# Optimization experiments

Hardware: AMD Instinct MI355X
Metric: run time of the kernel (lower is better)

Reference implementation:

```python
import jax, jax.numpy as jnp
import numpy as np

H, W = 4096, 4096
KH, KW = 11, 11


def setup_inputs() -> dict:
    key = jax.random.key(0)
    k1, k2 = jax.random.split(key)
    x = jax.random.normal(k1, (H, W), dtype=jnp.float32)
    weight = jax.random.uniform(k2, (KH, KW), dtype=jnp.float32)
    bias = jnp.zeros((1,), dtype=jnp.float32)
    return {"x": x, "weight": weight, "bias": bias}


def reference(x, weight, bias):
    # corr2d: valid 2D cross-correlation of a single-channel image with a
    # single kernel, then add scalar bias. Output shape [H-KH+1, W-KW+1].
    out = jax.lax.conv_general_dilated(
        x[None, None, :, :],            # NCHW, N=C=1
        weight[None, None, :, :],       # OIHW, O=I=1
        window_strides=(1, 1),
        padding="VALID",
        dimension_numbers=("NCHW", "OIHW", "NCHW"),
    )[0, 0]
    return out + bias[0]
```

## Files before the change

### kernel.cpp

```cpp
#include <hip/hip_runtime.h>
#include <hip/hip_bf16.h>

#define IH 4096
#define IW 4096
#define KH 11
#define KW 11
#define OH (IH - KH + 1)
#define OW (IW - KW + 1)

#define SROWS   26
#define TSTRIDE 84
#define NCHW    20
#define WCHUNK  (SROWS * NCHW)
#define TILE_SHORTS (SROWS * TSTRIDE)

#define STRIPS_X 64
#define ROWS_Y   256
#define NBLK     (STRIPS_X * ROWS_Y)

typedef short bf16x4 __attribute__((ext_vector_type(4)));
typedef short bf16x8 __attribute__((ext_vector_type(8)));
typedef float f32x4  __attribute__((ext_vector_type(4)));

__device__ __forceinline__ short f2b(float f) {
    __hip_bfloat16 h = __float2bfloat16(f);
    return __builtin_bit_cast(short, h);
}

__global__ void build_bmat(const float* __restrict__ w, short* __restrict__ bm) {
    const int tid = threadIdx.x;
#pragma unroll
    for (int t = 0; t < 22; ++t) {
        const int idx = tid + t * 256;
        const int kh = idx >> 9;
        const int j  = (idx >> 5) & 15;
        const int k  = idx & 31;
        const int d  = k - j;
        const float val = (d >= 0 && d < KW) ? w[kh * KW + d] : 0.f;
        bm[idx] = f2b(val);
    }
}

__global__ __launch_bounds__(64)
void conv2d_1w(const float* __restrict__ x,
               const short* __restrict__ bg,
               const float* __restrict__ bias,
               float* __restrict__ out) {
    __shared__ short tile[TILE_SHORTS];

    const int lane = threadIdx.x;
    const int g    = lane >> 4;
    const int li   = lane & 15;

    const int id    = (blockIdx.x & 7) * (NBLK / 8) + (blockIdx.x >> 3);
    const int strip = id >> 8;
    const int ty    = id & 255;
    const int gx0   = strip * 64;
    const int gy0   = ty * 16;

    const short* bp = bg + li * 32 + g * 8;
#define BLOAD(KH) const bf16x8 B##KH = *reinterpret_cast<const bf16x8*>(bp + (KH) * 512)
    BLOAD(0); BLOAD(1); BLOAD(2); BLOAD(3); BLOAD(4); BLOAD(5);
    BLOAD(6); BLOAD(7); BLOAD(8); BLOAD(9); BLOAD(10);
#undef BLOAD

#pragma unroll
    for (int it = 0; it < 9; ++it) {
        const int i = lane + it * 64;
        if (i < WCHUNK) {
            const int r  = i / NCHW;
            const int c4 = i - r * NCHW;
            const int gy = gy0 + r;
            const int gx = gx0 + c4 * 4;
            float4 v = make_float4(0.f, 0.f, 0.f, 0.f);
            if (gy < IH && gx + 3 < IW) {
                v = *reinterpret_cast<const float4*>(x + (size_t)gy * IW + gx);
            }
            bf16x4 b = { f2b(v.x), f2b(v.y), f2b(v.z), f2b(v.w) };
            *reinterpret_cast<bf16x4*>(&tile[r * TSTRIDE + c4 * 4]) = b;
        }
    }

    f32x4 acc[4] = {};
    const short* ap = &tile[li * TSTRIDE + g * 8];

    bf16x8 Ae[4], Ao[4];
#define LOADA(A, ROW) do {                                                   \
        const short* p_ = ap + (ROW) * TSTRIDE;                              \
        _Pragma("unroll")                                                    \
        for (int c = 0; c < 4; ++c) {                                        \
            bf16x4 lo = *reinterpret_cast<const bf16x4*>(p_ + c * 16);       \
            bf16x4 hi = *reinterpret_cast<const bf16x4*>(p_ + c * 16 + 4);   \
            A[c] = __builtin_shufflevector(lo, hi, 0, 1, 2, 3, 4, 5, 6, 7);  \
        }                                                                    \
    } while (0)
#define MFMA4(A, B) do {                                                     \
        _Pragma("unroll")                                                    \
        for (int c = 0; c < 4; ++c)                                          \
            acc[c] = __builtin_amdgcn_mfma_f32_16x16x32_bf16(A[c], B,        \
                                                             acc[c], 0, 0, 0); \
    } while (0)
#define STEPE(KH, B) LOADA(Ao, (KH) + 1); MFMA4(Ae, B); \
        __builtin_amdgcn_sched_barrier(0)
#define STEPO(KH, B) LOADA(Ae, (KH) + 1); MFMA4(Ao, B); \
        __builtin_amdgcn_sched_barrier(0)

    LOADA(Ae, 0);
    STEPE(0, B0);  STEPO(1, B1);  STEPE(2, B2);  STEPO(3, B3);
    STEPE(4, B4);  STEPO(5, B5);  STEPE(6, B6);  STEPO(7, B7);
    STEPE(8, B8);  STEPO(9, B9);  MFMA4(Ae, B10);

#undef STEPE
#undef STEPO
#undef MFMA4
#undef LOADA

    const float bv = bias[0];
#pragma unroll
    for (int c = 0; c < 4; ++c) {
        const int ox = gx0 + c * 16 + li;
        if (ox < OW) {
#pragma unroll
            for (int r = 0; r < 4; ++r) {
                const int oy = gy0 + g * 4 + r;
                if (oy < OH) {
                    out[(size_t)oy * OW + ox] = acc[c][r] + bv;
                }
            }
        }
    }
}

extern "C" void kernel_launch(void* const* d_in, const int* in_sizes, int n_in,
                              void* d_out, int out_size, void* d_ws, size_t ws_size,
                              hipStream_t stream) {
    const float* x    = (const float*)d_in[0];
    const float* w    = (const float*)d_in[1];
    const float* bias = (const float*)d_in[2];
    float* out        = (float*)d_out;
    short* bm         = (short*)d_ws;

    build_bmat<<<dim3(1), dim3(256), 0, stream>>>(w, bm);

    dim3 grid(NBLK);
    dim3 block(64);
    conv2d_1w<<<grid, block, 0, stream>>>(x, bm, bias, out);
}
```

Baseline: 44.37 us.

## Use async global-to-LDS loads with double-buffered 64x64 tiles per block

Replaces the one-wave 16-row strip kernel with 512-thread blocks that each process two adjacent 64x64 output tiles. Input rows are staged as fp32 directly into LDS with global_load_lds, and the second tile's load overlaps the first tile's MFMA compute. The bf16 conversion moves to the LDS read path. Larger tiles cut the halo re-read overhead (74 rows per 64 instead of 26 per 16), at the cost of twice the LDS footprint from fp32 storage, conversion work inside the inner loop, and fewer blocks overall.

Measured after the change: 40.43 us. 1.1x faster.

```diff
diff --git a/kernel.cpp b/kernel.cpp
--- a/kernel.cpp
+++ b/kernel.cpp
@@ -8,17 +8,17 @@
 #define OH (IH - KH + 1)
 #define OW (IW - KW + 1)
 
-#define SROWS   26
-#define TSTRIDE 84
-#define NCHW    20
-#define WCHUNK  (SROWS * NCHW)
-#define TILE_SHORTS (SROWS * TSTRIDE)
+#define BM 64
+#define BN 64
+#define TROWS   74
+#define FSTRIDE 84
+#define NCH_ROW 21
+#define NCHUNK  (TROWS * NCH_ROW)
+#define TILE_FLOATS (TROWS * FSTRIDE)
 
-#define STRIPS_X 64
-#define ROWS_Y   256
-#define NBLK     (STRIPS_X * ROWS_Y)
+#define TILES_X 64
+#define NPAIR   2048
 
-typedef short bf16x4 __attribute__((ext_vector_type(4)));
 typedef short bf16x8 __attribute__((ext_vector_type(8)));
 typedef float f32x4  __attribute__((ext_vector_type(4)));
 
@@ -41,94 +41,115 @@
     }
 }
 
-__global__ __launch_bounds__(64)
-void conv2d_1w(const float* __restrict__ x,
-               const short* __restrict__ bg,
-               const float* __restrict__ bias,
-               float* __restrict__ out) {
-    __shared__ short tile[TILE_SHORTS];
+__global__ __launch_bounds__(512)
+void conv2d_async(const float* __restrict__ x,
+                  const short* __restrict__ bg,
+                  const float* __restrict__ bias,
+                  float* __restrict__ out) {
+    __shared__ float buf[2][TILE_FLOATS];
 
-    const int lane = threadIdx.x;
+    const int tid = threadIdx.x;
+    const int pair = (blockIdx.x & 7) * (NPAIR / 8) + (blockIdx.x >> 3);
+    const int t0   = pair * 2;
+    const int gy0  = (t0 >> 6) * BM;
+    const int gxb  = (t0 & (TILES_X - 1)) * BN;
+
+    const int lane = tid & 63;
+    const int wvb  = tid & ~63;
+    const int wv   = tid >> 6;
+    const int wr   = wv >> 1;
+    const int ch   = wv & 1;
     const int g    = lane >> 4;
     const int li   = lane & 15;
-
-    const int id    = (blockIdx.x & 7) * (NBLK / 8) + (blockIdx.x >> 3);
-    const int strip = id >> 8;
-    const int ty    = id & 255;
-    const int gx0   = strip * 64;
-    const int gy0   = ty * 16;
+    const float bv = bias[0];
 
     const short* bp = bg + li * 32 + g * 8;
-#define BLOAD(KH) const bf16x8 B##KH = *reinterpret_cast<const bf16x8*>(bp + (KH) * 512)
+#define BLOAD(K) const bf16x8 B##K = *reinterpret_cast<const bf16x8*>(bp + (K) * 512)
     BLOAD(0); BLOAD(1); BLOAD(2); BLOAD(3); BLOAD(4); BLOAD(5);
     BLOAD(6); BLOAD(7); BLOAD(8); BLOAD(9); BLOAD(10);
 #undef BLOAD
 
-#pragma unroll
-    for (int it = 0; it < 9; ++it) {
-        const int i = lane + it * 64;
-        if (i < WCHUNK) {
-            const int r  = i / NCHW;
-            const int c4 = i - r * NCHW;
-            const int gy = gy0 + r;
-            const int gx = gx0 + c4 * 4;
-            float4 v = make_float4(0.f, 0.f, 0.f, 0.f);
-            if (gy < IH && gx + 3 < IW) {
-                v = *reinterpret_cast<const float4*>(x + (size_t)gy * IW + gx);
-            }
-            bf16x4 b = { f2b(v.x), f2b(v.y), f2b(v.z), f2b(v.w) };
-            *reinterpret_cast<bf16x4*>(&tile[r * TSTRIDE + c4 * 4]) = b;
-        }
-    }
-
-    f32x4 acc[4] = {};
-    const short* ap = &tile[li * TSTRIDE + g * 8];
-
-    bf16x8 Ae[4], Ao[4];
-#define LOADA(A, ROW) do {                                                   \
-        const short* p_ = ap + (ROW) * TSTRIDE;                              \
+#define DMAST(BI, GX0) do {                                                  \
         _Pragma("unroll")                                                    \
-        for (int c = 0; c < 4; ++c) {                                        \
-            bf16x4 lo = *reinterpret_cast<const bf16x4*>(p_ + c * 16);       \
-            bf16x4 hi = *reinterpret_cast<const bf16x4*>(p_ + c * 16 + 4);   \
-            A[c] = __builtin_shufflevector(lo, hi, 0, 1, 2, 3, 4, 5, 6, 7);  \
+        for (int it_ = 0; it_ < 4; ++it_) {                                  \
+            const int i_ = tid + it_ * 512;                                  \
+            if (i_ < NCHUNK) {                                               \
+                const int r_  = i_ / NCH_ROW;                                \
+                const int c4_ = i_ - r_ * NCH_ROW;                           \
+                const int gy_ = gy0 + r_;                                    \
+                const int gx_ = (GX0) + c4_ * 4;                             \
+                const float* s_ = (c4_ < 20 && gy_ < IH && gx_ + 3 < IW)     \
+                                  ? (x + (size_t)gy_ * IW + gx_) : x;        \
+                __builtin_amdgcn_global_load_lds(                            \
+                    (const __attribute__((address_space(1))) void*)s_,      \
+                    (__attribute__((address_space(3))) void*)                \
+                        &buf[BI][(it_ * 512 + wvb) * 4],                     \
+                    16, 0, 0);                                               \
+            }                                                                \
         }                                                                    \
     } while (0)
-#define MFMA4(A, B) do {                                                     \
+
+#define LOADA(A, ROW) do {                                                   \
         _Pragma("unroll")                                                    \
-        for (int c = 0; c < 4; ++c)                                          \
-            acc[c] = __builtin_amdgcn_mfma_f32_16x16x32_bf16(A[c], B,        \
-                                                             acc[c], 0, 0, 0); \
+        for (int c_ = 0; c_ < 2; ++c_) {                                     \
+            f32x4 p_ = *reinterpret_cast<const f32x4*>(ap + (ROW) * FSTRIDE + c_ * 16);     \
+            f32x4 q_ = *reinterpret_cast<const f32x4*>(ap + (ROW) * FSTRIDE + c_ * 16 + 4); \
+            bf16x8 v_;                                                       \
+            _Pragma("unroll")                                                \
+            for (int e_ = 0; e_ < 4; ++e_) {                                 \
+                v_[e_] = f2b(p_[e_]); v_[4 + e_] = f2b(q_[e_]);              \
+            }                                                                \
+            A[c_] = v_;                                                      \
+        }                                                                    \
     } while (0)
-#define STEPE(KH, B) LOADA(Ao, (KH) + 1); MFMA4(Ae, B); \
+#define MFMA2(A, BF) do {                                                    \
+        _Pragma("unroll")                                                    \
+        for (int c_ = 0; c_ < 2; ++c_)                                       \
+            acc[c_] = __builtin_amdgcn_mfma_f32_16x16x32_bf16(A[c_], (BF),   \
+                                                              acc[c_], 0, 0, 0); \
+    } while (0)
+#define STEPE(K, BF) LOADA(Ao, (K) + 1); MFMA2(Ae, BF); \
         __builtin_amdgcn_sched_barrier(0)
-#define STEPO(KH, B) LOADA(Ae, (KH) + 1); MFMA4(Ao, B); \
+#define STEPO(K, BF) LOADA(Ae, (K) + 1); MFMA2(Ao, BF); \
         __builtin_amdgcn_sched_barrier(0)
 
-    LOADA(Ae, 0);
-    STEPE(0, B0);  STEPO(1, B1);  STEPE(2, B2);  STEPO(3, B3);
-    STEPE(4, B4);  STEPO(5, B5);  STEPE(6, B6);  STEPO(7, B7);
-    STEPE(8, B8);  STEPO(9, B9);  MFMA4(Ae, B10);
+#define COMPUTE(BI, GX0) do {                                                \
+        f32x4 acc[2] = {};                                                   \
+        const float* ap = &buf[BI][(16 * wr + li) * FSTRIDE + ch * 32 + g * 8]; \
+        bf16x8 Ae[2], Ao[2];                                                 \
+        LOADA(Ae, 0);                                                        \
+        STEPE(0, B0); STEPO(1, B1); STEPE(2, B2); STEPO(3, B3);              \
+        STEPE(4, B4); STEPO(5, B5); STEPE(6, B6); STEPO(7, B7);              \
+        STEPE(8, B8); STEPO(9, B9); MFMA2(Ae, B10);                          \
+        _Pragma("unroll")                                                    \
+        for (int c_ = 0; c_ < 2; ++c_) {                                     \
+            const int ox_ = (GX0) + ch * 32 + c_ * 16 + li;                  \
+            if (ox_ < OW) {                                                  \
+                _Pragma("unroll")                                            \
+                for (int r_ = 0; r_ < 4; ++r_) {                             \
+                    const int oy_ = gy0 + wr * 16 + g * 4 + r_;              \
+                    if (oy_ < OH)                                            \
+                        out[(size_t)oy_ * OW + ox_] = acc[c_][r_] + bv;      \
+                }                                                            \
+            }                                                                \
+        }                                                                    \
+    } while (0)
 
+    DMAST(0, gxb);
+    __syncthreads();
+
+    DMAST(1, gxb + BN);
+    COMPUTE(0, gxb);
+    __syncthreads();
+
+    COMPUTE(1, gxb + BN);
+
+#undef COMPUTE
+#undef STEPO
 #undef STEPE
-#undef STEPO
-#undef MFMA4
+#undef MFMA2
 #undef LOADA
-
-    const float bv = bias[0];
-#pragma unroll
-    for (int c = 0; c < 4; ++c) {
-        const int ox = gx0 + c * 16 + li;
-        if (ox < OW) {
-#pragma unroll
-            for (int r = 0; r < 4; ++r) {
-                const int oy = gy0 + g * 4 + r;
-                if (oy < OH) {
-                    out[(size_t)oy * OW + ox] = acc[c][r] + bv;
-                }
-            }
-        }
-    }
+#undef DMAST
 }
 
 extern "C" void kernel_launch(void* const* d_in, const int* in_sizes, int n_in,
@@ -142,7 +163,7 @@
 
     build_bmat<<<dim3(1), dim3(256), 0, stream>>>(w, bm);
 
-    dim3 grid(NBLK);
-    dim3 block(64);
-    conv2d_1w<<<grid, block, 0, stream>>>(x, bm, bias, out);
+    dim3 grid(NPAIR);
+    dim3 block(512);
+    conv2d_async<<<grid, block, 0, stream>>>(x, bm, bias, out);
 }
```

## Share one 64x64 input tile across four waves to cut halo reloads

Applied to the files above, without the earlier changes.

Each block now has four waves that compute a 64x64 output tile from one shared bf16 staging tile of 74 rows, replacing single-wave 16-row strips that each reloaded a 10-row halo. This reduces redundant global reads of the input. The A-fragment pipeline switches to triple buffering with two rows prefetched ahead. It adds a block-wide barrier and larger blocks, which may reduce latency hiding per CU.

Measured after the change: 40.60 us. 8.5% less time.

```diff
diff --git a/kernel.cpp b/kernel.cpp
--- a/kernel.cpp
+++ b/kernel.cpp
@@ -8,15 +8,17 @@
 #define OH (IH - KH + 1)
 #define OW (IW - KW + 1)
 
-#define SROWS   26
+#define BM 64
+#define BN 64
+#define TROWS   74
 #define TSTRIDE 84
-#define NCHW    20
-#define WCHUNK  (SROWS * NCHW)
-#define TILE_SHORTS (SROWS * TSTRIDE)
+#define NC4     20
+#define NCHUNK  (TROWS * NC4)
+#define NITER   6
+#define TILE_SHORTS (TROWS * TSTRIDE)
 
-#define STRIPS_X 64
-#define ROWS_Y   256
-#define NBLK     (STRIPS_X * ROWS_Y)
+#define TILES_X 64
+#define NTILE   4096
 
 typedef short bf16x4 __attribute__((ext_vector_type(4)));
 typedef short bf16x8 __attribute__((ext_vector_type(8)));
@@ -41,35 +43,36 @@
     }
 }
 
-__global__ __launch_bounds__(64)
-void conv2d_1w(const float* __restrict__ x,
+__global__ __launch_bounds__(256)
+void conv2d_p3(const float* __restrict__ x,
                const short* __restrict__ bg,
                const float* __restrict__ bias,
                float* __restrict__ out) {
     __shared__ short tile[TILE_SHORTS];
 
-    const int lane = threadIdx.x;
+    const int tid = threadIdx.x;
+    const int blk = (blockIdx.x & 7) * (NTILE / 8) + (blockIdx.x >> 3);
+    const int gy0 = (blk >> 6) * BM;
+    const int gx0 = (blk & (TILES_X - 1)) * BN;
+
+    const int lane = tid & 63;
+    const int wv   = tid >> 6;
     const int g    = lane >> 4;
     const int li   = lane & 15;
-
-    const int id    = (blockIdx.x & 7) * (NBLK / 8) + (blockIdx.x >> 3);
-    const int strip = id >> 8;
-    const int ty    = id & 255;
-    const int gx0   = strip * 64;
-    const int gy0   = ty * 16;
+    const float bv = bias[0];
 
     const short* bp = bg + li * 32 + g * 8;
-#define BLOAD(KH) const bf16x8 B##KH = *reinterpret_cast<const bf16x8*>(bp + (KH) * 512)
+#define BLOAD(K) const bf16x8 B##K = *reinterpret_cast<const bf16x8*>(bp + (K) * 512)
     BLOAD(0); BLOAD(1); BLOAD(2); BLOAD(3); BLOAD(4); BLOAD(5);
     BLOAD(6); BLOAD(7); BLOAD(8); BLOAD(9); BLOAD(10);
 #undef BLOAD
 
 #pragma unroll
-    for (int it = 0; it < 9; ++it) {
-        const int i = lane + it * 64;
-        if (i < WCHUNK) {
-            const int r  = i / NCHW;
-            const int c4 = i - r * NCHW;
+    for (int it = 0; it < NITER; ++it) {
+        const int i = tid + it * 256;
+        if (i < NCHUNK) {
+            const int r  = i / NC4;
+            const int c4 = i - r * NC4;
             const int gy = gy0 + r;
             const int gx = gx0 + c4 * 4;
             float4 v = make_float4(0.f, 0.f, 0.f, 0.f);
@@ -80,11 +83,12 @@
             *reinterpret_cast<bf16x4*>(&tile[r * TSTRIDE + c4 * 4]) = b;
         }
     }
+    __syncthreads();
 
     f32x4 acc[4] = {};
-    const short* ap = &tile[li * TSTRIDE + g * 8];
+    const short* ap = &tile[(16 * wv + li) * TSTRIDE + g * 8];
 
-    bf16x8 Ae[4], Ao[4];
+    bf16x8 Aa[4], Ab[4], Ac[4];
 #define LOADA(A, ROW) do {                                                   \
         const short* p_ = ap + (ROW) * TSTRIDE;                              \
         _Pragma("unroll")                                                    \
@@ -100,29 +104,34 @@
             acc[c] = __builtin_amdgcn_mfma_f32_16x16x32_bf16(A[c], B,        \
                                                              acc[c], 0, 0, 0); \
     } while (0)
-#define STEPE(KH, B) LOADA(Ao, (KH) + 1); MFMA4(Ae, B); \
-        __builtin_amdgcn_sched_barrier(0)
-#define STEPO(KH, B) LOADA(Ae, (KH) + 1); MFMA4(Ao, B); \
+#define STEP(CUR, NXT, ROW, B) LOADA(NXT, ROW); MFMA4(CUR, B); \
         __builtin_amdgcn_sched_barrier(0)
 
-    LOADA(Ae, 0);
-    STEPE(0, B0);  STEPO(1, B1);  STEPE(2, B2);  STEPO(3, B3);
-    STEPE(4, B4);  STEPO(5, B5);  STEPE(6, B6);  STEPO(7, B7);
-    STEPE(8, B8);  STEPO(9, B9);  MFMA4(Ae, B10);
+    LOADA(Aa, 0);
+    LOADA(Ab, 1);
+    STEP(Aa, Ac, 2, B0);
+    STEP(Ab, Aa, 3, B1);
+    STEP(Ac, Ab, 4, B2);
+    STEP(Aa, Ac, 5, B3);
+    STEP(Ab, Aa, 6, B4);
+    STEP(Ac, Ab, 7, B5);
+    STEP(Aa, Ac, 8, B6);
+    STEP(Ab, Aa, 9, B7);
+    STEP(Ac, Ab, 10, B8);
+    MFMA4(Aa, B9);
+    MFMA4(Ab, B10);
 
-#undef STEPE
-#undef STEPO
+#undef STEP
 #undef MFMA4
 #undef LOADA
 
-    const float bv = bias[0];
 #pragma unroll
     for (int c = 0; c < 4; ++c) {
         const int ox = gx0 + c * 16 + li;
         if (ox < OW) {
 #pragma unroll
             for (int r = 0; r < 4; ++r) {
-                const int oy = gy0 + g * 4 + r;
+                const int oy = gy0 + wv * 16 + g * 4 + r;
                 if (oy < OH) {
                     out[(size_t)oy * OW + ox] = acc[c][r] + bv;
                 }
@@ -142,7 +151,7 @@
 
     build_bmat<<<dim3(1), dim3(256), 0, stream>>>(w, bm);
 
-    dim3 grid(NBLK);
-    dim3 block(64);
-    conv2d_1w<<<grid, block, 0, stream>>>(x, bm, bias, out);
+    dim3 grid(NTILE);
+    dim3 block(256);
+    conv2d_p3<<<grid, block, 0, stream>>>(x, bm, bias, out);
 }
```
